# Kernel tuning notes

Measured on AMD Instinct MI355X. Metric: run time of the kernel, lower is better.

Reference implementation:

```python
import jax, jax.numpy as jnp
import numpy as np

B, N, IN_DIM = 16, 256, 768
MEM, HID = 300, 64
NEG = -1e30
SLOPE = 0.01  # LeakyReLU negative slope


def setup_inputs() -> dict:
    key = jax.random.key(0)
    ks = jax.random.split(key, 8)
    # binary adjacency mask, float32 as in the torch module's mask_logits math
    adj = (jax.random.uniform(ks[0], (B, N, N)) < 0.3).astype(jnp.float32)
    feature = jax.random.normal(ks[1], (B, N, IN_DIM), jnp.float32)

    def lin(k, fan_in, shape):
        return (jax.random.normal(k, shape, jnp.float32) / np.sqrt(fan_in)).astype(jnp.float32)

    W0 = lin(ks[2], IN_DIM, (IN_DIM, MEM)); b0 = jnp.zeros((MEM,), jnp.float32)
    W1 = lin(ks[3], MEM, (MEM, MEM));       b1 = jnp.zeros((MEM,), jnp.float32)
    A1 = lin(ks[4], 2 * MEM, (2 * MEM, HID)); ab1 = jnp.zeros((HID,), jnp.float32)
    A2 = lin(ks[5], HID, (HID, 1));           ab2 = jnp.zeros((1,), jnp.float32)
    return dict(adj=adj, feature=feature, W0=W0, b0=b0, W1=W1, b1=b1,
                A1=A1, ab1=ab1, A2=A2, ab2=ab2)


def reference(adj, feature, W0, b0, W1, b1, A1, ab1, A2, ab2):
    Bn, Nn = adj.shape[0], adj.shape[1]
    # additive split of the concat-MLP first layer: A1 @ [h_i; h_j] = Wa@h_i + Wb@h_j
    Wa, Wb = A1[:MEM], A1[MEM:]
    a2 = A2[:, 0]
    x = feature
    for Wl, bl in ((W0, b0), (W1, b1)):  # num_layers = 2
        h = x @ Wl + bl                              # [B, N, MEM]
        si = h @ Wa                                  # [B, N, HID] (source half)
        sj = h @ Wb + ab1                            # [B, N, HID] (target half + bias)
        z = jax.nn.relu(si[:, :, None, :] + sj[:, None, :, :])  # [B, N, N, HID]
        e = jnp.einsum('bijh,h->bij', z, a2) + ab2[0]            # [B, N, N]
        e = jnp.where(e > 0, e, SLOPE * e)           # LeakyReLU(0.01)
        logits = e * adj + (1.0 - adj) * NEG         # mask_logits
        # faithful quirk: softmax over the FLATTENED N*N dimension
        att = jax.nn.softmax(logits.reshape(Bn, -1), axis=1).reshape(Bn, Nn, Nn)
        x = jnp.einsum('bij,bjd->bid', att, h)       # bmm aggregation
        # dropout is identity in eval mode
    return x
```

## Files before the change

### kernel.cpp

```cpp
#include <hip/hip_runtime.h>
#include <hip/hip_bf16.h>

static constexpr int Nc = 256;
static constexpr float NEGc = -1e30f;
static constexpr float SLOPEc = 0.01f;

using f32x4 = __attribute__((ext_vector_type(4))) float;
using s16x8 = __attribute__((ext_vector_type(8))) short;

__device__ __forceinline__ void mfma16(f32x4& d, s16x8 a, s16x8 b) {
    asm("v_mfma_f32_16x16x32_bf16 %0, %1, %2, %0" : "+v"(d) : "v"(a), "v"(b));
}

__device__ __forceinline__ void barrier_lds() {
    asm volatile("s_waitcnt lgkmcnt(0)\n\ts_barrier" ::: "memory");
}

__device__ __forceinline__ float wredMax(float v) {
#pragma unroll
    for (int o = 32; o; o >>= 1) v = fmaxf(v, __shfl_xor(v, o, 64));
    return v;
}
__device__ __forceinline__ float wredSum(float v) {
#pragma unroll
    for (int o = 32; o; o >>= 1) v += __shfl_xor(v, o, 64);
    return v;
}

__device__ __forceinline__ unsigned packhi(unsigned u1, unsigned u0) {
    return __builtin_amdgcn_perm(u1, u0, 0x07060302u);
}

__device__ __forceinline__ void do_wsplit(
    const float* __restrict__ src, int K, int ch, int c,
    ushort* __restrict__ dh, ushort* __restrict__ dl) {
    float v[8];
#pragma unroll
    for (int e = 0; e < 8; e++) {
        int k = ch * 8 + e;
        v[e] = (k < K && c < 300) ? src[(size_t)k * 300 + c] : 0.f;
    }
    unsigned hu[4], lu[4];
#pragma unroll
    for (int q = 0; q < 4; q++) {
        unsigned u0 = __float_as_uint(v[q * 2]);
        unsigned u1 = __float_as_uint(v[q * 2 + 1]);
        float r0 = v[q * 2] - __uint_as_float(u0 & 0xFFFF0000u);
        float r1 = v[q * 2 + 1] - __uint_as_float(u1 & 0xFFFF0000u);
        hu[q] = packhi(u1, u0);
        lu[q] = packhi(__float_as_uint(r1), __float_as_uint(r0));
    }
    size_t dst = ((size_t)ch * 448 + c) * 8;
    *(uint4*)&dh[dst] = make_uint4(hu[0], hu[1], hu[2], hu[3]);
    *(uint4*)&dl[dst] = make_uint4(lu[0], lu[1], lu[2], lu[3]);
}

__device__ __forceinline__ void do_wa(
    const float* __restrict__ Wsrc, int K, int k, int c,
    const float* __restrict__ A1,
    ushort* __restrict__ dh, ushort* __restrict__ dl) {
    float accv = 0.f;
    if (k < K) {
        const float* wrow = Wsrc + (size_t)k * 300;
        const float* a1c = (c < 64) ? (A1 + c) : (A1 + 300 * 64 + (c - 64));
        for (int mm = 0; mm < 300; mm += 4) {
            accv += wrow[mm] * a1c[(size_t)mm * 64]
                  + wrow[mm + 1] * a1c[(size_t)(mm + 1) * 64]
                  + wrow[mm + 2] * a1c[(size_t)(mm + 2) * 64]
                  + wrow[mm + 3] * a1c[(size_t)(mm + 3) * 64];
        }
    }
    unsigned u = __float_as_uint(accv);
    float r = accv - __uint_as_float(u & 0xFFFF0000u);
    size_t dst = ((size_t)(k >> 3) * 448 + 320 + c) * 8 + (k & 7);
    dh[dst] = (ushort)(u >> 16);
    dl[dst] = (ushort)(__float_as_uint(r) >> 16);
}

__device__ __forceinline__ void do_bias(
    const float* __restrict__ b, int col,
    const float* __restrict__ A1, const float* __restrict__ ab1,
    float* __restrict__ biasOut) {
    float v;
    if (col < 320) {
        v = (col < 300) ? b[col] : 0.f;
    } else {
        int cc = col - 320;
        const float* a1c = (cc < 64) ? (A1 + cc) : (A1 + 300 * 64 + (cc - 64));
        float s = 0.f;
        for (int mm = 0; mm < 300; mm++) s += b[mm] * a1c[(size_t)mm * 64];
        v = s + ((cc >= 64) ? ab1[cc - 64] : 0.f);
    }
    biasOut[col] = v;
}

__global__ void __launch_bounds__(256) convert0(
    const float* __restrict__ W0, const float* __restrict__ b0,
    const float* __restrict__ A1, const float* __restrict__ ab1,
    ushort* __restrict__ F0h, ushort* __restrict__ F0l,
    float* __restrict__ bias0) {
    int idx = blockIdx.x * 256 + threadIdx.x;
    if (idx >= 129472) return;
    if (idx < 30720) {
        do_wsplit(W0, 768, idx / 320, idx % 320, F0h, F0l);
    } else if (idx < 129024) {
        int i2 = idx - 30720;
        do_wa(W0, 768, i2 >> 7, i2 & 127, A1, F0h, F0l);
    } else {
        do_bias(b0, idx - 129024, A1, ab1, bias0);
    }
}

__device__ __forceinline__ void gemm_core(
    const float* __restrict__ Ab, const ushort* __restrict__ Whb,
    const ushort* __restrict__ Wlb, int WCOLS, int col0, int Kp,
    f32x4 (&acc)[2][2]) {
    __shared__ __align__(16) short Ah[2][2048], Al[2][2048];
    __shared__ __align__(16) short Bh[2][2048], Bl[2][2048];
    const int tid = threadIdx.x;
    const int lane = tid & 63, wave = tid >> 6;
    const int wm = wave >> 1, wn = wave & 1;
    const int m = lane & 15, kch = lane >> 4;
    const int arow = tid >> 2, aoff = (tid & 3) * 8;
    const int bchunk = tid >> 6, bcol = tid & 63;
    const int bsel = (bchunk * 64 + bcol) * 8;

    float fa[8];
    s16x8 bhv, blv;

    auto loadrg = [&](int kk) {
        *(float4*)&fa[0] = *(const float4*)(Ab + kk);
        *(float4*)&fa[4] = *(const float4*)(Ab + kk + 4);
        size_t boff = (size_t)((kk >> 3) + bchunk) * WCOLS * 8
                    + (size_t)(col0 + bcol) * 8;
        bhv = *(const s16x8*)(Whb + boff);
        blv = *(const s16x8*)(Wlb + boff);
    };
    auto stage = [&](int buf) {
#pragma unroll
        for (int q = 0; q < 2; q++) {
            unsigned u0 = __float_as_uint(fa[q * 4 + 0]);
            unsigned u1 = __float_as_uint(fa[q * 4 + 1]);
            unsigned u2 = __float_as_uint(fa[q * 4 + 2]);
            unsigned u3 = __float_as_uint(fa[q * 4 + 3]);
            float r0 = fa[q * 4 + 0] - __uint_as_float(u0 & 0xFFFF0000u);
            float r1 = fa[q * 4 + 1] - __uint_as_float(u1 & 0xFFFF0000u);
            float r2 = fa[q * 4 + 2] - __uint_as_float(u2 & 0xFFFF0000u);
            float r3 = fa[q * 4 + 3] - __uint_as_float(u3 & 0xFFFF0000u);
            uint2 th, tl;
            th.x = packhi(u1, u0); th.y = packhi(u3, u2);
            tl.x = packhi(__float_as_uint(r1), __float_as_uint(r0));
            tl.y = packhi(__float_as_uint(r3), __float_as_uint(r2));
            int kq = aoff + q * 4;
            int base = ((kq >> 3) * 64 + arow) * 8 + (kq & 7);
            *(uint2*)&Ah[buf][base] = th;
            *(uint2*)&Al[buf][base] = tl;
        }
        *(s16x8*)&Bh[buf][bsel] = bhv;
        *(s16x8*)&Bl[buf][bsel] = blv;
    };

    loadrg(0);
    stage(0);
    if (Kp > 32) loadrg(32);
    barrier_lds();

    for (int k0 = 0; k0 < Kp; k0 += 32) {
        const int cur = (k0 >> 5) & 1;
        s16x8 Afh[2], Afl[2], Bfh[2], Bfl[2];
#pragma unroll
        for (int fr = 0; fr < 2; fr++) {
            int off = (kch * 64 + wm * 32 + fr * 16 + m) * 8;
            Afh[fr] = *(const s16x8*)&Ah[cur][off];
            Afl[fr] = *(const s16x8*)&Al[cur][off];
        }
#pragma unroll
        for (int fc = 0; fc < 2; fc++) {
            int off = ((kch << 6) + wn * 32 + fc * 16 + m) * 8;
            Bfh[fc] = *(const s16x8*)&Bh[cur][off];
            Bfl[fc] = *(const s16x8*)&Bl[cur][off];
        }
        if (k0 + 32 < Kp) {
            stage(cur ^ 1);
            if (k0 + 64 < Kp) loadrg(k0 + 64);
        }
#pragma unroll
        for (int fr = 0; fr < 2; fr++)
#pragma unroll
            for (int fc = 0; fc < 2; fc++) {
                mfma16(acc[fr][fc], Afh[fr], Bfh[fc]);
                mfma16(acc[fr][fc], Afl[fr], Bfh[fc]);
                mfma16(acc[fr][fc], Afh[fr], Bfl[fc]);
            }
        barrier_lds();
    }
}

template<bool FC>
__global__ void __launch_bounds__(256) xf_kernel(
    const float* __restrict__ X, int Kp,
    const ushort* __restrict__ Fh, const ushort* __restrict__ Fl,
    const float* __restrict__ bias,
    ushort* __restrict__ Hh, ushort* __restrict__ Hl,
    float* __restrict__ si, float* __restrict__ sjT,
    const float* __restrict__ W1, const float* __restrict__ b1,
    const float* __restrict__ A1, const float* __restrict__ ab1,
    ushort* __restrict__ F1h, ushort* __restrict__ F1l,
    float* __restrict__ bias1) {
    if (FC && blockIdx.x >= 448) {
        int idx = (blockIdx.x - 448) * 256 + threadIdx.x;
        if (idx >= 54208) return;
        if (idx < 12800) {
            do_wsplit(W1, 300, idx / 320, idx % 320, F1h, F1l);
        } else if (idx < 53760) {
            int i2 = idx - 12800;
            do_wa(W1, 300, i2 >> 7, i2 & 127, A1, F1h, F1l);
        } else {
            do_bias(b1, idx - 53760, A1, ab1, bias1);
        }
        return;
    }
    const int tid = threadIdx.x;
    const int lane = tid & 63, wave = tid >> 6;
    const int wm = wave >> 1, wn = wave & 1;
    const int m = lane & 15, kch = lane >> 4;
    const int bid = blockIdx.x;
    const int col0 = (bid % 7) * 64, row0 = (bid / 7) * 64;

    f32x4 acc[2][2];
#pragma unroll
    for (int i = 0; i < 2; i++)
#pragma unroll
        for (int j = 0; j < 2; j++)
#pragma unroll
            for (int e = 0; e < 4; e++) acc[i][j][e] = 0.f;

    const float* Ab = X + (size_t)(row0 + (tid >> 2)) * Kp + (tid & 3) * 8;
    gemm_core(Ab, Fh, Fl, 448, col0, Kp, acc);
    asm volatile("s_nop 7\ns_nop 7\ns_nop 7" ::);

#pragma unroll
    for (int fr = 0; fr < 2; fr++) {
        int rbase = row0 + wm * 32 + fr * 16 + (kch << 2);
#pragma unroll
        for (int fc = 0; fc < 2; fc++) {
            int col = col0 + wn * 32 + fc * 16 + m;
            float bv = bias[col];
            float vv[4];
#pragma unroll
            for (int e = 0; e < 4; e++) vv[e] = acc[fr][fc][e] + bv;
            if (col < 320) {
                unsigned u0 = __float_as_uint(vv[0]);
                unsigned u1 = __float_as_uint(vv[1]);
                unsigned u2 = __float_as_uint(vv[2]);
                unsigned u3 = __float_as_uint(vv[3]);
                float r0 = vv[0] - __uint_as_float(u0 & 0xFFFF0000u);
                float r1 = vv[1] - __uint_as_float(u1 & 0xFFFF0000u);
                float r2 = vv[2] - __uint_as_float(u2 & 0xFFFF0000u);
                float r3 = vv[3] - __uint_as_float(u3 & 0xFFFF0000u);
                uint2 th, tl;
                th.x = packhi(u1, u0); th.y = packhi(u3, u2);
                tl.x = packhi(__float_as_uint(r1), __float_as_uint(r0));
                tl.y = packhi(__float_as_uint(r3), __float_as_uint(r2));
                int k = rbase & 255, bb = rbase >> 8;
                size_t dst = (size_t)bb * 81920 + ((size_t)(k >> 3) * 320 + col) * 8 + (k & 7);
                *(uint2*)&Hh[dst] = th;
                *(uint2*)&Hl[dst] = tl;
            } else if (col < 384) {
                int cc = col - 320;
#pragma unroll
                for (int e = 0; e < 4; e++)
                    si[(size_t)(rbase + e) * 64 + cc] = vv[e];
            } else {
                int cc = col - 384;
                int bb = rbase >> 8, j0 = rbase & 255;
                float4 v4 = make_float4(vv[0], vv[1], vv[2], vv[3]);
                *(float4*)&sjT[((size_t)(bb * 64 + cc)) * Nc + j0] = v4;
            }
        }
    }
}

__global__ void __launch_bounds__(256) scores_kernel(
    const float* __restrict__ si, const float* __restrict__ sjT,
    const float* __restrict__ adj, const float* __restrict__ A2,
    const float* __restrict__ ab2p,
    float* __restrict__ P, float* __restrict__ rmx, float* __restrict__ rsm) {
    int b = blockIdx.x, ic = blockIdx.y;
    const int j = threadIdx.x;
    __shared__ __align__(16) float sis[8][68];
    __shared__ __align__(16) float a2s[64];
    __shared__ __align__(16) float E[8][260];

    if (j < 64) a2s[j] = A2[j];
#pragma unroll
    for (int idx = j, t = 0; t < 2; t++, idx += 256) {
        int r = idx >> 6, h = idx & 63;
        sis[r][h] = si[(size_t)(b * Nc + ic * 8 + r) * 64 + h];
    }
    float sv[64];
    const float* sjb = sjT + ((size_t)b << 6) * Nc + j;
#pragma unroll
    for (int h = 0; h < 64; h++) sv[h] = sjb[(size_t)h * Nc];
    __syncthreads();

    float acc[8] = {};
#pragma unroll
    for (int hq = 0; hq < 16; hq++) {
        float4 a2q = *(const float4*)&a2s[hq * 4];
#pragma unroll
        for (int r = 0; r < 8; r++) {
            const float4 siq = *(const float4*)&sis[r][hq * 4];
            acc[r] += a2q.x * fmaxf(siq.x + sv[hq * 4 + 0], 0.f)
                    + a2q.y * fmaxf(siq.y + sv[hq * 4 + 1], 0.f)
                    + a2q.z * fmaxf(siq.z + sv[hq * 4 + 2], 0.f)
                    + a2q.w * fmaxf(siq.w + sv[hq * 4 + 3], 0.f);
        }
    }
    float ab2v = ab2p[0];
    const float* adjp = adj + (size_t)(b * Nc + ic * 8) * Nc + j;
#pragma unroll
    for (int r = 0; r < 8; r++) {
        float e = acc[r] + ab2v;
        e = e > 0.f ? e : SLOPEc * e;
        float a = adjp[(size_t)r * Nc];
        E[r][j] = (a != 0.f) ? e : NEGc;
    }
    __syncthreads();
    int wv = j >> 6, lane = j & 63;
#pragma unroll
    for (int rr = 0; rr < 2; rr++) {
        int r = wv * 2 + rr;
        float4 q = *(const float4*)&E[r][lane * 4];
        float m4 = fmaxf(fmaxf(q.x, q.y), fmaxf(q.z, q.w));
        float rm = wredMax(m4);
        float4 p;
        p.x = expf(q.x - rm); p.y = expf(q.y - rm);
        p.z = expf(q.z - rm); p.w = expf(q.w - rm);
        float rs = wredSum(p.x + p.y + p.z + p.w);
        int gi = ic * 8 + r;
        *(float4*)(P + (size_t)(b * Nc + gi) * Nc + lane * 4) = p;
        if (lane == 0) { rmx[b * Nc + gi] = rm; rsm[b * Nc + gi] = rs; }
    }
}

__global__ void __launch_bounds__(256) pv_kernel(
    const float* __restrict__ P,
    const ushort* __restrict__ Hh, const ushort* __restrict__ Hl,
    const float* __restrict__ rmx, const float* __restrict__ rsm,
    float* __restrict__ out, int OS) {
    __shared__ float sclS[256];
    __shared__ float mb[4], sb[4];
    const int tid = threadIdx.x;
    const int lane = tid & 63, wave = tid >> 6;
    const int col0 = blockIdx.x * 64, row0 = blockIdx.y * 64;
    const int b = blockIdx.z;

    {
        float mv = rmx[b * 256 + tid];
        float wmx = wredMax(mv);
        if (!lane) mb[wave] = wmx;
        __syncthreads();
        float M = fmaxf(fmaxf(mb[0], mb[1]), fmaxf(mb[2], mb[3]));
        float ex = expf(mv - M);
        float ws = wredSum(rsm[b * 256 + tid] * ex);
        if (!lane) sb[wave] = ws;
        __syncthreads();
        float S = sb[0] + sb[1] + sb[2] + sb[3];
        sclS[tid] = ex / S;
    }

    f32x4 acc[2][2];
#pragma unroll
    for (int i = 0; i < 2; i++)
#pragma unroll
        for (int j = 0; j < 2; j++)
#pragma unroll
            for (int e = 0; e < 4; e++) acc[i][j][e] = 0.f;

    const float* Ab = P + (size_t)b * 65536 + (size_t)(row0 + (tid >> 2)) * Nc + (tid & 3) * 8;
    gemm_core(Ab, Hh + (size_t)b * 81920, Hl + (size_t)b * 81920, 320, col0, 256, acc);
    asm volatile("s_nop 7\ns_nop 7\ns_nop 7" ::);

    const int wm = wave >> 1, wn = wave & 1;
    const int m = lane & 15, kch = lane >> 4;
    float* ob = out + (size_t)b * 256 * OS;
#pragma unroll
    for (int fr = 0; fr < 2; fr++) {
        int rbase = row0 + wm * 32 + fr * 16 + (kch << 2);
#pragma unroll
        for (int fc = 0; fc < 2; fc++) {
            int col = col0 + wn * 32 + fc * 16 + m;
            if (col < OS) {
#pragma unroll
                for (int e = 0; e < 4; e++)
                    ob[(size_t)(rbase + e) * OS + col] = acc[fr][fc][e] * sclS[rbase + e];
            }
        }
    }
}

extern "C" void kernel_launch(void* const* d_in, const int* in_sizes, int n_in,
                              void* d_out, int out_size, void* d_ws, size_t ws_size,
                              hipStream_t stream) {
    const float* adj     = (const float*)d_in[0];
    const float* feature = (const float*)d_in[1];
    const float* W0      = (const float*)d_in[2];
    const float* b0      = (const float*)d_in[3];
    const float* W1      = (const float*)d_in[4];
    const float* b1      = (const float*)d_in[5];
    const float* A1      = (const float*)d_in[6];
    const float* ab1     = (const float*)d_in[7];
    const float* A2      = (const float*)d_in[8];
    const float* ab2     = (const float*)d_in[9];

    char* ws = (char*)d_ws;
    float*  x1    = (float*)(ws);
    float*  si    = (float*)(ws + 5242880);
    float*  sjT   = (float*)(ws + 6291456);
    float*  P     = (float*)(ws + 7340032);
    float*  rmx   = (float*)(ws + 11534336);
    float*  rsm   = (float*)(ws + 11550720);
    float*  bias0 = (float*)(ws + 11567104);
    float*  bias1 = (float*)(ws + 11568896);
    ushort* F0h   = (ushort*)(ws + 11570688);
    ushort* F0l   = (ushort*)(ws + 12258816);
    ushort* F1h   = (ushort*)(ws + 12946944);
    ushort* F1l   = (ushort*)(ws + 13233664);
    ushort* Hh    = (ushort*)(ws + 13520384);
    ushort* Hl    = (ushort*)(ws + 16141824);
    float* outp   = (float*)d_out;

    convert0<<<506, 256, 0, stream>>>(W0, b0, A1, ab1, F0h, F0l, bias0);

    xf_kernel<true><<<660, 256, 0, stream>>>(
        feature, 768, F0h, F0l, bias0, Hh, Hl, si, sjT,
        W1, b1, A1, ab1, F1h, F1l, bias1);
    scores_kernel<<<dim3(16, 32), 256, 0, stream>>>(
        si, sjT, adj, A2, ab2, P, rmx, rsm);
    pv_kernel<<<dim3(5, 4, 16), 256, 0, stream>>>(
        P, Hh, Hl, rmx, rsm, x1, 320);

    xf_kernel<false><<<448, 256, 0, stream>>>(
        x1, 320, F1h, F1l, bias1, Hh, Hl, si, sjT,
        nullptr, nullptr, nullptr, nullptr, nullptr, nullptr, nullptr);
    scores_kernel<<<dim3(16, 32), 256, 0, stream>>>(
        si, sjT, adj, A2, ab2, P, rmx, rsm);
    pv_kernel<<<dim3(5, 4, 16), 256, 0, stream>>>(
        P, Hh, Hl, rmx, rsm, outp, 300);
}
```

Before: 94.84 us.

## Replace LDS-staged GEMM core with direct global-to-register fragment loads

The shared-memory double-buffered GEMM core is replaced by a version where each wave loads its own A rows and pre-split B fragments from global memory straight into registers, with two register stages for software pipelining. This drops LDS staging and the per-iteration barriers, and the inline-asm MFMA is replaced by the compiler builtin so the scheduler can interleave it. In exchange, A rows are re-read by both column waves and each wave re-splits A into bf16 hi/lo, which adds redundant global traffic and VALU work. A __syncthreads is added after the softmax scale write, since the shared scale array is now read without any barrier from the GEMM.

```diff
diff --git a/kernel.cpp b/kernel.cpp
--- a/kernel.cpp
+++ b/kernel.cpp
@@ -6,14 +6,10 @@
 static constexpr float SLOPEc = 0.01f;
 
 using f32x4 = __attribute__((ext_vector_type(4))) float;
-using s16x8 = __attribute__((ext_vector_type(8))) short;
-
-__device__ __forceinline__ void mfma16(f32x4& d, s16x8 a, s16x8 b) {
-    asm("v_mfma_f32_16x16x32_bf16 %0, %1, %2, %0" : "+v"(d) : "v"(a), "v"(b));
-}
-
-__device__ __forceinline__ void barrier_lds() {
-    asm volatile("s_waitcnt lgkmcnt(0)\n\ts_barrier" ::: "memory");
+using bf16x8 = __attribute__((ext_vector_type(8))) __bf16;
+
+__device__ __forceinline__ void mfma16(f32x4& d, bf16x8 a, bf16x8 b) {
+    d = __builtin_amdgcn_mfma_f32_16x16x32_bf16(a, b, d, 0, 0, 0);
 }
 
 __device__ __forceinline__ float wredMax(float v) {
@@ -111,88 +107,85 @@
     }
 }
 
-__device__ __forceinline__ void gemm_core(
-    const float* __restrict__ Ab, const ushort* __restrict__ Whb,
-    const ushort* __restrict__ Wlb, int WCOLS, int col0, int Kp,
-    f32x4 (&acc)[2][2]) {
-    __shared__ __align__(16) short Ah[2][2048], Al[2][2048];
-    __shared__ __align__(16) short Bh[2][2048], Bl[2][2048];
-    const int tid = threadIdx.x;
-    const int lane = tid & 63, wave = tid >> 6;
+struct ABregs {
+    float a0[8], a1[8];
+    bf16x8 b0h, b0l, b1h, b1l;
+};
+
+__device__ __forceinline__ void rr_load(
+    ABregs& S, const float* __restrict__ Ar0, const float* __restrict__ Ar1,
+    const ushort* __restrict__ B0h, const ushort* __restrict__ B0l,
+    const ushort* __restrict__ B1h, const ushort* __restrict__ B1l,
+    int WCOLS, int k0) {
+    *(float4*)&S.a0[0] = *(const float4*)(Ar0 + k0);
+    *(float4*)&S.a0[4] = *(const float4*)(Ar0 + k0 + 4);
+    *(float4*)&S.a1[0] = *(const float4*)(Ar1 + k0);
+    *(float4*)&S.a1[4] = *(const float4*)(Ar1 + k0 + 4);
+    size_t bo = (size_t)(k0 >> 3) * WCOLS * 8;
+    S.b0h = *(const bf16x8*)(B0h + bo);
+    S.b0l = *(const bf16x8*)(B0l + bo);
+    S.b1h = *(const bf16x8*)(B1h + bo);
+    S.b1l = *(const bf16x8*)(B1l + bo);
+}
+
+__device__ __forceinline__ void splitfrag(const float* a, bf16x8& hi, bf16x8& lo) {
+    union { uint4 u; bf16x8 v; } H, L;
+    unsigned hu[4], lu[4];
+#pragma unroll
+    for (int q = 0; q < 4; q++) {
+        unsigned u0 = __float_as_uint(a[2 * q]);
+        unsigned u1 = __float_as_uint(a[2 * q + 1]);
+        float r0 = a[2 * q] - __uint_as_float(u0 & 0xFFFF0000u);
+        float r1 = a[2 * q + 1] - __uint_as_float(u1 & 0xFFFF0000u);
+        hu[q] = packhi(u1, u0);
+        lu[q] = packhi(__float_as_uint(r1), __float_as_uint(r0));
+    }
+    H.u = make_uint4(hu[0], hu[1], hu[2], hu[3]);
+    L.u = make_uint4(lu[0], lu[1], lu[2], lu[3]);
+    hi = H.v; lo = L.v;
+}
+
+__device__ __forceinline__ void rr_compute(const ABregs& S, f32x4 (&acc)[2][2]) {
+    bf16x8 A0h, A0l, A1h, A1l;
+    splitfrag(S.a0, A0h, A0l);
+    splitfrag(S.a1, A1h, A1l);
+    mfma16(acc[0][0], A0h, S.b0h);
+    mfma16(acc[0][0], A0l, S.b0h);
+    mfma16(acc[0][0], A0h, S.b0l);
+    mfma16(acc[0][1], A0h, S.b1h);
+    mfma16(acc[0][1], A0l, S.b1h);
+    mfma16(acc[0][1], A0h, S.b1l);
+    mfma16(acc[1][0], A1h, S.b0h);
+    mfma16(acc[1][0], A1l, S.b0h);
+    mfma16(acc[1][0], A1h, S.b0l);
+    mfma16(acc[1][1], A1h, S.b1h);
+    mfma16(acc[1][1], A1l, S.b1h);
+    mfma16(acc[1][1], A1h, S.b1l);
+}
+
+__device__ __forceinline__ void gemm_rr(
+    const float* __restrict__ Abase, int AS,
+    const ushort* __restrict__ Bh, const ushort* __restrict__ Bl,
+    int WCOLS, int col0, int Kp, f32x4 (&acc)[2][2]) {
+    const int lane = threadIdx.x & 63, wave = threadIdx.x >> 6;
     const int wm = wave >> 1, wn = wave & 1;
     const int m = lane & 15, kch = lane >> 4;
-    const int arow = tid >> 2, aoff = (tid & 3) * 8;
-    const int bchunk = tid >> 6, bcol = tid & 63;
-    const int bsel = (bchunk * 64 + bcol) * 8;
-
-    float fa[8];
-    s16x8 bhv, blv;
-
-    auto loadrg = [&](int kk) {
-        *(float4*)&fa[0] = *(const float4*)(Ab + kk);
-        *(float4*)&fa[4] = *(const float4*)(Ab + kk + 4);
-        size_t boff = (size_t)((kk >> 3) + bchunk) * WCOLS * 8
-                    + (size_t)(col0 + bcol) * 8;
-        bhv = *(const s16x8*)(Whb + boff);
-        blv = *(const s16x8*)(Wlb + boff);
-    };
-    auto stage = [&](int buf) {
-#pragma unroll
-        for (int q = 0; q < 2; q++) {
-            unsigned u0 = __float_as_uint(fa[q * 4 + 0]);
-            unsigned u1 = __float_as_uint(fa[q * 4 + 1]);
-            unsigned u2 = __float_as_uint(fa[q * 4 + 2]);
-            unsigned u3 = __float_as_uint(fa[q * 4 + 3]);
-            float r0 = fa[q * 4 + 0] - __uint_as_float(u0 & 0xFFFF0000u);
-            float r1 = fa[q * 4 + 1] - __uint_as_float(u1 & 0xFFFF0000u);
-            float r2 = fa[q * 4 + 2] - __uint_as_float(u2 & 0xFFFF0000u);
-            float r3 = fa[q * 4 + 3] - __uint_as_float(u3 & 0xFFFF0000u);
-            uint2 th, tl;
-            th.x = packhi(u1, u0); th.y = packhi(u3, u2);
-            tl.x = packhi(__float_as_uint(r1), __float_as_uint(r0));
-            tl.y = packhi(__float_as_uint(r3), __float_as_uint(r2));
-            int kq = aoff + q * 4;
-            int base = ((kq >> 3) * 64 + arow) * 8 + (kq & 7);
-            *(uint2*)&Ah[buf][base] = th;
-            *(uint2*)&Al[buf][base] = tl;
-        }
-        *(s16x8*)&Bh[buf][bsel] = bhv;
-        *(s16x8*)&Bl[buf][bsel] = blv;
-    };
-
-    loadrg(0);
-    stage(0);
-    if (Kp > 32) loadrg(32);
-    barrier_lds();
-
-    for (int k0 = 0; k0 < Kp; k0 += 32) {
-        const int cur = (k0 >> 5) & 1;
-        s16x8 Afh[2], Afl[2], Bfh[2], Bfl[2];
-#pragma unroll
-        for (int fr = 0; fr < 2; fr++) {
-            int off = (kch * 64 + wm * 32 + fr * 16 + m) * 8;
-            Afh[fr] = *(const s16x8*)&Ah[cur][off];
-            Afl[fr] = *(const s16x8*)&Al[cur][off];
-        }
-#pragma unroll
-        for (int fc = 0; fc < 2; fc++) {
-            int off = ((kch << 6) + wn * 32 + fc * 16 + m) * 8;
-            Bfh[fc] = *(const s16x8*)&Bh[cur][off];
-            Bfl[fc] = *(const s16x8*)&Bl[cur][off];
-        }
-        if (k0 + 32 < Kp) {
-            stage(cur ^ 1);
-            if (k0 + 64 < Kp) loadrg(k0 + 64);
-        }
-#pragma unroll
-        for (int fr = 0; fr < 2; fr++)
-#pragma unroll
-            for (int fc = 0; fc < 2; fc++) {
-                mfma16(acc[fr][fc], Afh[fr], Bfh[fc]);
-                mfma16(acc[fr][fc], Afl[fr], Bfh[fc]);
-                mfma16(acc[fr][fc], Afh[fr], Bfl[fc]);
-            }
-        barrier_lds();
+    const float* Ar0 = Abase + (size_t)(wm * 32 + m) * AS + kch * 8;
+    const float* Ar1 = Ar0 + (size_t)16 * AS;
+    size_t bbase = ((size_t)kch * WCOLS + col0 + wn * 32 + m) * 8;
+    const ushort* B0h = Bh + bbase;
+    const ushort* B0l = Bl + bbase;
+    const ushort* B1h = B0h + 16 * 8;
+    const ushort* B1l = B0l + 16 * 8;
+
+    ABregs P, Q;
+    rr_load(P, Ar0, Ar1, B0h, B0l, B1h, B1l, WCOLS, 0);
+    for (int k0 = 0; k0 < Kp; k0 += 64) {
+        rr_load(Q, Ar0, Ar1, B0h, B0l, B1h, B1l, WCOLS, k0 + 32);
+        rr_compute(P, acc);
+        if (k0 + 64 < Kp)
+            rr_load(P, Ar0, Ar1, B0h, B0l, B1h, B1l, WCOLS, k0 + 64);
+        rr_compute(Q, acc);
     }
 }
 
@@ -235,9 +228,7 @@
 #pragma unroll
             for (int e = 0; e < 4; e++) acc[i][j][e] = 0.f;
 
-    const float* Ab = X + (size_t)(row0 + (tid >> 2)) * Kp + (tid & 3) * 8;
-    gemm_core(Ab, Fh, Fl, 448, col0, Kp, acc);
-    asm volatile("s_nop 7\ns_nop 7\ns_nop 7" ::);
+    gemm_rr(X + (size_t)row0 * Kp, Kp, Fh, Fl, 448, col0, Kp, acc);
 
 #pragma unroll
     for (int fr = 0; fr < 2; fr++) {
@@ -368,6 +359,7 @@
         __syncthreads();
         float S = sb[0] + sb[1] + sb[2] + sb[3];
         sclS[tid] = ex / S;
+        __syncthreads();
     }
 
     f32x4 acc[2][2];
@@ -378,9 +370,9 @@
 #pragma unroll
             for (int e = 0; e < 4; e++) acc[i][j][e] = 0.f;
 
-    const float* Ab = P + (size_t)b * 65536 + (size_t)(row0 + (tid >> 2)) * Nc + (tid & 3) * 8;
-    gemm_core(Ab, Hh + (size_t)b * 81920, Hl + (size_t)b * 81920, 320, col0, 256, acc);
-    asm volatile("s_nop 7\ns_nop 7\ns_nop 7" ::);
+    gemm_rr(P + (size_t)b * 65536 + (size_t)row0 * Nc, Nc,
+            Hh + (size_t)b * 81920, Hl + (size_t)b * 81920,
+            320, col0, 256, acc);
 
     const int wm = wave >> 1, wn = wave & 1;
     const int m = lane & 15, kch = lane >> 4;
```

Measured after the change: 120.4 us. 27.0% more time.

## Fuse score softmax with P·V aggregation and defer normalization to next layer

Applied to the files above, without the earlier changes.

Merges the scores and PV kernels into one kernel. Each block computes 16 rows of attention logits, exponentiates them, splits them into bf16 hi/lo pairs held in swizzled LDS, and immediately multiplies them against H with MFMA, so the P matrix is never written to global memory. The global flattened-softmax scale is then applied later: for layer 1 it is folded into the A-operand staging of the next xf GEMM, and for layer 2 a small scale_out kernel applies it. This removes the P round trip and one launch per layer, but the fused kernel has only 256 blocks, each wave reloads B fragments straight from global memory, and an extra pass over the output is added.

```diff
diff --git a/kernel.cpp b/kernel.cpp
--- a/kernel.cpp
+++ b/kernel.cpp
@@ -7,9 +7,13 @@
 
 using f32x4 = __attribute__((ext_vector_type(4))) float;
 using s16x8 = __attribute__((ext_vector_type(8))) short;
+using bf16x8 = __attribute__((ext_vector_type(8))) __bf16;
 
 __device__ __forceinline__ void mfma16(f32x4& d, s16x8 a, s16x8 b) {
     asm("v_mfma_f32_16x16x32_bf16 %0, %1, %2, %0" : "+v"(d) : "v"(a), "v"(b));
+}
+__device__ __forceinline__ void mfma16b(f32x4& d, bf16x8 a, bf16x8 b) {
+    d = __builtin_amdgcn_mfma_f32_16x16x32_bf16(a, b, d, 0, 0, 0);
 }
 
 __device__ __forceinline__ void barrier_lds() {
@@ -111,10 +115,11 @@
     }
 }
 
+template<bool SCA>
 __device__ __forceinline__ void gemm_core(
-    const float* __restrict__ Ab, const ushort* __restrict__ Whb,
-    const ushort* __restrict__ Wlb, int WCOLS, int col0, int Kp,
-    f32x4 (&acc)[2][2]) {
+    const float* __restrict__ Ab, float sA,
+    const ushort* __restrict__ Whb, const ushort* __restrict__ Wlb,
+    int WCOLS, int col0, int Kp, f32x4 (&acc)[2][2]) {
     __shared__ __align__(16) short Ah[2][2048], Al[2][2048];
     __shared__ __align__(16) short Bh[2][2048], Bl[2][2048];
     const int tid = threadIdx.x;
@@ -139,14 +144,17 @@
     auto stage = [&](int buf) {
 #pragma unroll
         for (int q = 0; q < 2; q++) {
-            unsigned u0 = __float_as_uint(fa[q * 4 + 0]);
-            unsigned u1 = __float_as_uint(fa[q * 4 + 1]);
-            unsigned u2 = __float_as_uint(fa[q * 4 + 2]);
-            unsigned u3 = __float_as_uint(fa[q * 4 + 3]);
-            float r0 = fa[q * 4 + 0] - __uint_as_float(u0 & 0xFFFF0000u);
-            float r1 = fa[q * 4 + 1] - __uint_as_float(u1 & 0xFFFF0000u);
-            float r2 = fa[q * 4 + 2] - __uint_as_float(u2 & 0xFFFF0000u);
-            float r3 = fa[q * 4 + 3] - __uint_as_float(u3 & 0xFFFF0000u);
+            float f0 = fa[q * 4 + 0], f1 = fa[q * 4 + 1];
+            float f2 = fa[q * 4 + 2], f3 = fa[q * 4 + 3];
+            if constexpr (SCA) { f0 *= sA; f1 *= sA; f2 *= sA; f3 *= sA; }
+            unsigned u0 = __float_as_uint(f0);
+            unsigned u1 = __float_as_uint(f1);
+            unsigned u2 = __float_as_uint(f2);
+            unsigned u3 = __float_as_uint(f3);
+            float r0 = f0 - __uint_as_float(u0 & 0xFFFF0000u);
+            float r1 = f1 - __uint_as_float(u1 & 0xFFFF0000u);
+            float r2 = f2 - __uint_as_float(u2 & 0xFFFF0000u);
+            float r3 = f3 - __uint_as_float(u3 & 0xFFFF0000u);
             uint2 th, tl;
             th.x = packhi(u1, u0); th.y = packhi(u3, u2);
             tl.x = packhi(__float_as_uint(r1), __float_as_uint(r0));
@@ -206,7 +214,8 @@
     const float* __restrict__ W1, const float* __restrict__ b1,
     const float* __restrict__ A1, const float* __restrict__ ab1,
     ushort* __restrict__ F1h, ushort* __restrict__ F1l,
-    float* __restrict__ bias1) {
+    float* __restrict__ bias1,
+    const float* __restrict__ rmx, const float* __restrict__ rsm) {
     if (FC && blockIdx.x >= 448) {
         int idx = (blockIdx.x - 448) * 256 + threadIdx.x;
         if (idx >= 54208) return;
@@ -227,6 +236,27 @@
     const int bid = blockIdx.x;
     const int col0 = (bid % 7) * 64, row0 = (bid / 7) * 64;
 
+    float sA = 1.0f;
+    if constexpr (!FC) {
+        __shared__ float sclS[256];
+        __shared__ float mb[4], sb[4];
+        const int b = (bid / 7) >> 2;
+        float mv = rmx[b * 256 + tid];
+        float wmx = wredMax(mv);
+        if (!lane) mb[wave] = wmx;
+        __syncthreads();
+        float M = fmaxf(fmaxf(mb[0], mb[1]), fmaxf(mb[2], mb[3]));
+        float ex = expf(mv - M);
+        float ws = wredSum(rsm[b * 256 + tid] * ex);
+        if (!lane) sb[wave] = ws;
+        __syncthreads();
+        float S = sb[0] + sb[1] + sb[2] + sb[3];
+        sclS[tid] = ex / S;
+        __syncthreads();
+        sA = sclS[(row0 + (tid >> 2)) & 255];
+        __syncthreads();
+    }
+
     f32x4 acc[2][2];
 #pragma unroll
     for (int i = 0; i < 2; i++)
@@ -236,7 +266,7 @@
             for (int e = 0; e < 4; e++) acc[i][j][e] = 0.f;
 
     const float* Ab = X + (size_t)(row0 + (tid >> 2)) * Kp + (tid & 3) * 8;
-    gemm_core(Ab, Fh, Fl, 448, col0, Kp, acc);
+    gemm_core<!FC>(Ab, sA, Fh, Fl, 448, col0, Kp, acc);
     asm volatile("s_nop 7\ns_nop 7\ns_nop 7" ::);
 
 #pragma unroll
@@ -281,22 +311,27 @@
     }
 }
 
-__global__ void __launch_bounds__(256) scores_kernel(
+__global__ void __launch_bounds__(256) spv_kernel(
     const float* __restrict__ si, const float* __restrict__ sjT,
     const float* __restrict__ adj, const float* __restrict__ A2,
     const float* __restrict__ ab2p,
-    float* __restrict__ P, float* __restrict__ rmx, float* __restrict__ rsm) {
-    int b = blockIdx.x, ic = blockIdx.y;
+    const ushort* __restrict__ Hh, const ushort* __restrict__ Hl,
+    float* __restrict__ rmx, float* __restrict__ rsm,
+    float* __restrict__ outO) {
+    const int b = blockIdx.x, ic = blockIdx.y;
     const int j = threadIdx.x;
-    __shared__ __align__(16) float sis[8][68];
+    const int gi0 = ic * 16;
+    __shared__ __align__(16) float sis[16][68];
     __shared__ __align__(16) float a2s[64];
-    __shared__ __align__(16) float E[8][260];
+    __shared__ __align__(16) float E[16][260];
+    __shared__ __align__(16) ushort PhL[4096], PlL[4096];
 
     if (j < 64) a2s[j] = A2[j];
 #pragma unroll
-    for (int idx = j, t = 0; t < 2; t++, idx += 256) {
+    for (int t = 0; t < 4; t++) {
+        int idx = j + t * 256;
         int r = idx >> 6, h = idx & 63;
-        sis[r][h] = si[(size_t)(b * Nc + ic * 8 + r) * 64 + h];
+        sis[r][h] = si[(size_t)(b * Nc + gi0 + r) * 64 + h];
     }
     float sv[64];
     const float* sjb = sjT + ((size_t)b << 6) * Nc + j;
@@ -304,99 +339,132 @@
     for (int h = 0; h < 64; h++) sv[h] = sjb[(size_t)h * Nc];
     __syncthreads();
 
-    float acc[8] = {};
-#pragma unroll
+    float acc[16] = {};
+#pragma unroll 4
     for (int hq = 0; hq < 16; hq++) {
         float4 a2q = *(const float4*)&a2s[hq * 4];
-#pragma unroll
-        for (int r = 0; r < 8; r++) {
+        float s0 = sv[hq * 4 + 0], s1 = sv[hq * 4 + 1];
+        float s2 = sv[hq * 4 + 2], s3 = sv[hq * 4 + 3];
+#pragma unroll
+        for (int r = 0; r < 16; r++) {
             const float4 siq = *(const float4*)&sis[r][hq * 4];
-            acc[r] += a2q.x * fmaxf(siq.x + sv[hq * 4 + 0], 0.f)
-                    + a2q.y * fmaxf(siq.y + sv[hq * 4 + 1], 0.f)
-                    + a2q.z * fmaxf(siq.z + sv[hq * 4 + 2], 0.f)
-                    + a2q.w * fmaxf(siq.w + sv[hq * 4 + 3], 0.f);
+            acc[r] += a2q.x * fmaxf(siq.x + s0, 0.f)
+                    + a2q.y * fmaxf(siq.y + s1, 0.f)
+                    + a2q.z * fmaxf(siq.z + s2, 0.f)
+                    + a2q.w * fmaxf(siq.w + s3, 0.f);
         }
     }
     float ab2v = ab2p[0];
-    const float* adjp = adj + (size_t)(b * Nc + ic * 8) * Nc + j;
-#pragma unroll
-    for (int r = 0; r < 8; r++) {
+    const float* adjp = adj + (size_t)(b * Nc + gi0) * Nc + j;
+#pragma unroll
+    for (int r = 0; r < 16; r++) {
         float e = acc[r] + ab2v;
         e = e > 0.f ? e : SLOPEc * e;
         float a = adjp[(size_t)r * Nc];
         E[r][j] = (a != 0.f) ? e : NEGc;
     }
     __syncthreads();
-    int wv = j >> 6, lane = j & 63;
-#pragma unroll
-    for (int rr = 0; rr < 2; rr++) {
-        int r = wv * 2 + rr;
-        float4 q = *(const float4*)&E[r][lane * 4];
-        float m4 = fmaxf(fmaxf(q.x, q.y), fmaxf(q.z, q.w));
-        float rm = wredMax(m4);
-        float4 p;
-        p.x = expf(q.x - rm); p.y = expf(q.y - rm);
-        p.z = expf(q.z - rm); p.w = expf(q.w - rm);
-        float rs = wredSum(p.x + p.y + p.z + p.w);
-        int gi = ic * 8 + r;
-        *(float4*)(P + (size_t)(b * Nc + gi) * Nc + lane * 4) = p;
-        if (lane == 0) { rmx[b * Nc + gi] = rm; rsm[b * Nc + gi] = rs; }
-    }
-}
-
-__global__ void __launch_bounds__(256) pv_kernel(
-    const float* __restrict__ P,
-    const ushort* __restrict__ Hh, const ushort* __restrict__ Hl,
-    const float* __restrict__ rmx, const float* __restrict__ rsm,
-    float* __restrict__ out, int OS) {
+    {
+        const int wv = j >> 6, lane = j & 63;
+#pragma unroll
+        for (int rr = 0; rr < 4; rr++) {
+            int r = wv * 4 + rr;
+            float4 q = *(const float4*)&E[r][lane * 4];
+            float m4 = fmaxf(fmaxf(q.x, q.y), fmaxf(q.z, q.w));
+            float rm = wredMax(m4);
+            float4 p;
+            p.x = expf(q.x - rm); p.y = expf(q.y - rm);
+            p.z = expf(q.z - rm); p.w = expf(q.w - rm);
+            float rs = wredSum(p.x + p.y + p.z + p.w);
+            unsigned u0 = __float_as_uint(p.x), u1 = __float_as_uint(p.y);
+            unsigned u2 = __float_as_uint(p.z), u3 = __float_as_uint(p.w);
+            float r0 = p.x - __uint_as_float(u0 & 0xFFFF0000u);
+            float r1 = p.y - __uint_as_float(u1 & 0xFFFF0000u);
+            float r2 = p.z - __uint_as_float(u2 & 0xFFFF0000u);
+            float r3 = p.w - __uint_as_float(u3 & 0xFFFF0000u);
+            int sidx = r * 256 + ((lane * 4) ^ ((r & 7) << 3));
+            *(uint2*)&PhL[sidx] = make_uint2(packhi(u1, u0), packhi(u3, u2));
+            *(uint2*)&PlL[sidx] = make_uint2(
+                packhi(__float_as_uint(r1), __float_as_uint(r0)),
+                packhi(__float_as_uint(r3), __float_as_uint(r2)));
+            if (lane == 0) {
+                rmx[b * Nc + gi0 + r] = rm;
+                rsm[b * Nc + gi0 + r] = rs;
+            }
+        }
+    }
+    __syncthreads();
+
+    const int lane = j & 63, wave = j >> 6;
+    const int m = lane & 15, kch = lane >> 4;
+    const int ar = lane & 15;
+    const int colb = wave * 80;
+    const ushort* HhB = Hh + (size_t)b * 81920;
+    const ushort* HlB = Hl + (size_t)b * 81920;
+
+    f32x4 o[5];
+#pragma unroll
+    for (int fc = 0; fc < 5; fc++)
+#pragma unroll
+        for (int e = 0; e < 4; e++) o[fc][e] = 0.f;
+
+#pragma unroll
+    for (int ks = 0; ks < 8; ks++) {
+        const int j0 = ks * 32;
+        int ai = ar * 256 + ((j0 + kch * 8) ^ ((ar & 7) << 3));
+        bf16x8 Ah = *(const bf16x8*)&PhL[ai];
+        bf16x8 Al = *(const bf16x8*)&PlL[ai];
+#pragma unroll
+        for (int fc = 0; fc < 5; fc++) {
+            int col = colb + fc * 16 + m;
+            size_t bo = (size_t)((j0 >> 3) + kch) * 2560 + (size_t)col * 8;
+            bf16x8 Bh = *(const bf16x8*)(HhB + bo);
+            bf16x8 Bl = *(const bf16x8*)(HlB + bo);
+            mfma16b(o[fc], Ah, Bh);
+            mfma16b(o[fc], Al, Bh);
+            mfma16b(o[fc], Ah, Bl);
+        }
+    }
+    float* ob = outO + (size_t)(b * Nc + gi0) * 320;
+#pragma unroll
+    for (int fc = 0; fc < 5; fc++) {
+        int col = colb + fc * 16 + m;
+#pragma unroll
+        for (int e = 0; e < 4; e++) {
+            int row = kch * 4 + e;
+            ob[(size_t)row * 320 + col] = o[fc][e];
+        }
+    }
+}
+
+__global__ void __launch_bounds__(256) scale_out(
+    const float* __restrict__ o1, const float* __restrict__ rmx,
+    const float* __restrict__ rsm, float* __restrict__ out) {
+    const int b = blockIdx.x, t16 = blockIdx.y;
+    const int tid = threadIdx.x;
+    const int lane = tid & 63, wave = tid >> 6;
     __shared__ float sclS[256];
     __shared__ float mb[4], sb[4];
-    const int tid = threadIdx.x;
-    const int lane = tid & 63, wave = tid >> 6;
-    const int col0 = blockIdx.x * 64, row0 = blockIdx.y * 64;
-    const int b = blockIdx.z;
-
-    {
-        float mv = rmx[b * 256 + tid];
-        float wmx = wredMax(mv);
-        if (!lane) mb[wave] = wmx;
-        __syncthreads();
-        float M = fmaxf(fmaxf(mb[0], mb[1]), fmaxf(mb[2], mb[3]));
-        float ex = expf(mv - M);
-        float ws = wredSum(rsm[b * 256 + tid] * ex);
-        if (!lane) sb[wave] = ws;
-        __syncthreads();
-        float S = sb[0] + sb[1] + sb[2] + sb[3];
-        sclS[tid] = ex / S;
-    }
-
-    f32x4 acc[2][2];
-#pragma unroll
-    for (int i = 0; i < 2; i++)
-#pragma unroll
-        for (int j = 0; j < 2; j++)
-#pragma unroll
-            for (int e = 0; e < 4; e++) acc[i][j][e] = 0.f;
-
-    const float* Ab = P + (size_t)b * 65536 + (size_t)(row0 + (tid >> 2)) * Nc + (tid & 3) * 8;
-    gemm_core(Ab, Hh + (size_t)b * 81920, Hl + (size_t)b * 81920, 320, col0, 256, acc);
-    asm volatile("s_nop 7\ns_nop 7\ns_nop 7" ::);
-
-    const int wm = wave >> 1, wn = wave & 1;
-    const int m = lane & 15, kch = lane >> 4;
-    float* ob = out + (size_t)b * 256 * OS;
-#pragma unroll
-    for (int fr = 0; fr < 2; fr++) {
-        int rbase = row0 + wm * 32 + fr * 16 + (kch << 2);
-#pragma unroll
-        for (int fc = 0; fc < 2; fc++) {
-            int col = col0 + wn * 32 + fc * 16 + m;
-            if (col < OS) {
-#pragma unroll
-                for (int e = 0; e < 4; e++)
-                    ob[(size_t)(rbase + e) * OS + col] = acc[fr][fc][e] * sclS[rbase + e];
-            }
-        }
+    float mv = rmx[b * 256 + tid];
+    float wmx = wredMax(mv);
+    if (!lane) mb[wave] = wmx;
+    __syncthreads();
+    float M = fmaxf(fmaxf(mb[0], mb[1]), fmaxf(mb[2], mb[3]));
+    float ex = expf(mv - M);
+    float ws = wredSum(rsm[b * 256 + tid] * ex);
+    if (!lane) sb[wave] = ws;
+    __syncthreads();
+    float S = sb[0] + sb[1] + sb[2] + sb[3];
+    sclS[tid] = ex / S;
+    __syncthreads();
+#pragma unroll
+    for (int r = 0; r < 16; r++) {
+        int gi = t16 * 16 + r;
+        float s = sclS[gi];
+        const float* src = o1 + (size_t)(b * 256 + gi) * 320;
+        float* dst = out + (size_t)(b * 256 + gi) * 300;
+        for (int c = tid; c < 300; c += 256)
+            dst[c] = src[c] * s;
     }
 }
 
@@ -418,34 +486,32 @@
     float*  x1    = (float*)(ws);
     float*  si    = (float*)(ws + 5242880);
     float*  sjT   = (float*)(ws + 6291456);
-    float*  P     = (float*)(ws + 7340032);
-    float*  rmx   = (float*)(ws + 11534336);
-    float*  rsm   = (float*)(ws + 11550720);
-    float*  bias0 = (float*)(ws + 11567104);
-    float*  bias1 = (float*)(ws + 11568896);
-    ushort* F0h   = (ushort*)(ws + 11570688);
-    ushort* F0l   = (ushort*)(ws + 12258816);
-    ushort* F1h   = (ushort*)(ws + 12946944);
-    ushort* F1l   = (ushort*)(ws + 13233664);
-    ushort* Hh    = (ushort*)(ws + 13520384);
-    ushort* Hl    = (ushort*)(ws + 16141824);
+    float*  o1    = (float*)(ws + 7340032);
+    float*  rmx   = (float*)(ws + 12582912);
+    float*  rsm   = (float*)(ws + 12599296);
+    float*  bias0 = (float*)(ws + 12615680);
+    float*  bias1 = (float*)(ws + 12617472);
+    ushort* F0h   = (ushort*)(ws + 12619264);
+    ushort* F0l   = (ushort*)(ws + 13307392);
+    ushort* F1h   = (ushort*)(ws + 13995520);
+    ushort* F1l   = (ushort*)(ws + 14282240);
+    ushort* Hh    = (ushort*)(ws + 14568960);
+    ushort* Hl    = (ushort*)(ws + 17190400);
     float* outp   = (float*)d_out;
 
     convert0<<<506, 256, 0, stream>>>(W0, b0, A1, ab1, F0h, F0l, bias0);
 
     xf_kernel<true><<<660, 256, 0, stream>>>(
         feature, 768, F0h, F0l, bias0, Hh, Hl, si, sjT,
-        W1, b1, A1, ab1, F1h, F1l, bias1);
-    scores_kernel<<<dim3(16, 32), 256, 0, stream>>>(
-        si, sjT, adj, A2, ab2, P, rmx, rsm);
-    pv_kernel<<<dim3(5, 4, 16), 256, 0, stream>>>(
-        P, Hh, Hl, rmx, rsm, x1, 320);
+        W1, b1, A1, ab1, F1h, F1l, bias1, nullptr, nullptr);
+    spv_kernel<<<dim3(16, 16), 256, 0, stream>>>(
+        si, sjT, adj, A2, ab2, Hh, Hl, rmx, rsm, x1);
 
     xf_kernel<false><<<448, 256, 0, stream>>>(
         x1, 320, F1h, F1l, bias1, Hh, Hl, si, sjT,
-        nullptr, nullptr, nullptr, nullptr, nullptr, nullptr, nullptr);
-    scores_kernel<<<dim3(16, 32), 256, 0, stream>>>(
-        si, sjT, adj, A2, ab2, P, rmx, rsm);
-    pv_kernel<<<dim3(5, 4, 16), 256, 0, stream>>>(
-        P, Hh, Hl, rmx, rsm, outp, 300);
-}
+        nullptr, nullptr, nullptr, nullptr, nullptr, nullptr, nullptr,
+        rmx, rsm);
+    spv_kernel<<<dim3(16, 16), 256, 0, stream>>>(
+        si, sjT, adj, A2, ab2, Hh, Hl, rmx, rsm, o1);
+    scale_out<<<dim3(16, 16), 256, 0, stream>>>(o1, rmx, rsm, outp);
+}
```

After: 123.3 us. 30.0% more time.
